# Performance work log

Hardware: AMD Instinct MI355X
Metric: run time of the kernel (lower is better)

## Reference

```python
import jax, jax.numpy as jnp
import numpy as np
import math

B, L, D, H = 2, 2048, 1024, 16
HD = D // H  # 64
SYNC_THRESHOLD = -0.7
LN_EPS = 1e-12


def setup_inputs() -> dict:
    key = jax.random.key(0)
    ks = jax.random.split(key, 12)
    s = 0.02
    return {
        "hidden_states": jax.random.normal(ks[0], (B, L, D), dtype=jnp.float32),
        "attention_mask": jnp.zeros((B, 1, 1, L), dtype=jnp.float32),
        "phi": jax.random.normal(ks[1], (B, L, H), dtype=jnp.float32),
        "Wq": jax.random.normal(ks[2], (D, D), dtype=jnp.float32) * s,
        "bq": jnp.zeros((D,), dtype=jnp.float32),
        "Wk": jax.random.normal(ks[3], (D, D), dtype=jnp.float32) * s,
        "bk": jnp.zeros((D,), dtype=jnp.float32),
        "Wv": jax.random.normal(ks[4], (D, D), dtype=jnp.float32) * s,
        "bv": jnp.zeros((D,), dtype=jnp.float32),
        "Wo": jax.random.normal(ks[5], (D, D), dtype=jnp.float32) * s,
        "bo": jnp.zeros((D,), dtype=jnp.float32),
        "ln_g": jnp.ones((D,), dtype=jnp.float32),
        "ln_b": jnp.zeros((D,), dtype=jnp.float32),
    }


def _shape(x):  # [B,L,D] -> [B,H,L,HD]
    return x.reshape(B, L, H, HD).transpose(0, 2, 1, 3)


def _rotate_half(x):
    x1, x2 = jnp.split(x, 2, axis=-1)
    return jnp.concatenate([-x2, x1], axis=-1)


def reference(hidden_states, attention_mask, phi, Wq, bq, Wk, bk, Wv, bv, Wo, bo, ln_g, ln_b):
    residual = hidden_states
    q = _shape(hidden_states @ Wq.T + bq)
    k = _shape(hidden_states @ Wk.T + bk)
    v = _shape(hidden_states @ Wv.T + bv)

    # phase per (batch, head, token): [B,H,L,1]; constant across head_dim,
    # so cos/sin of the concatenated phase are the same scalar per token/head.
    p = jnp.transpose(phi, (0, 2, 1))[..., None]
    cos_p = jnp.cos(p)
    sin_p = jnp.sin(p)
    q_rot = q * cos_p + _rotate_half(q) * sin_p
    k_rot = k * cos_p + _rotate_half(k) * sin_p

    scores = jnp.einsum("bhqd,bhkd->bhqk", q_rot, k_rot) / math.sqrt(HD)

    # data-dependent sync mask: mask pairs whose phase difference is anti-synced
    delta_phi = p - jnp.swapaxes(p, -1, -2)           # [B,H,L,L]
    eye = jnp.eye(L, dtype=bool)[None, None]          # [1,1,L,L]
    sync_mask = (jnp.cos(delta_phi) < SYNC_THRESHOLD) & ~eye
    scores = jnp.where(sync_mask, -1e9, scores)
    scores = scores + attention_mask

    # all-masked edge case: zero diagonal score so softmax attends to self
    row_max = jnp.max(scores, axis=-1, keepdims=True)
    all_masked = row_max <= -1e8
    scores = jnp.where(all_masked & eye, 0.0, scores)

    probs = jax.nn.softmax(scores, axis=-1)
    ctx = jnp.einsum("bhqk,bhkd->bhqd", probs, v)
    ctx = ctx.transpose(0, 2, 1, 3).reshape(B, L, D)

    out = ctx @ Wo.T + bo
    x = out + residual
    mean = jnp.mean(x, axis=-1, keepdims=True)
    var = jnp.var(x, axis=-1, keepdims=True)
    return (x - mean) / jnp.sqrt(var + LN_EPS) * ln_g + ln_b
```

## Files before the change

kernel.cpp:

```cpp
#include <hip/hip_runtime.h>
#include <cmath>

#define BB 2
#define LL 2048
#define DD 1024
#define HH 16
#define HDD 64

typedef _Float16 v8h __attribute__((ext_vector_type(8)));
typedef _Float16 v4h __attribute__((ext_vector_type(4)));
typedef _Float16 v2h __attribute__((ext_vector_type(2)));
typedef float v4f __attribute__((ext_vector_type(4)));

#define LOG2E 1.44269504089f
#define NEGB  (-1.442695e9f)
#define AMTHR (-1.442695e8f)

#define GLD(gp, lp)                                                        \
  __builtin_amdgcn_global_load_lds(                                        \
      (const __attribute__((address_space(1))) void*)(gp),                 \
      (__attribute__((address_space(3))) void*)(lp), 16, 0, 0)

__global__ __launch_bounds__(256) void cvt_all(
    const float* __restrict__ hs, const float* __restrict__ wq,
    const float* __restrict__ wk, const float* __restrict__ wv,
    const float* __restrict__ wo, _Float16* __restrict__ hsh,
    _Float16* __restrict__ wqkvh, _Float16* __restrict__ woh)
{
  const int i = blockIdx.x * 256 + threadIdx.x;
  const float* s;
  _Float16* d;
  if (i < 1048576)      { s = hs + (size_t)i * 4;            d = hsh + (size_t)i * 4; }
  else if (i < 1310720) { int j = i - 1048576; s = wq + (size_t)j * 4; d = wqkvh + (size_t)j * 4; }
  else if (i < 1572864) { int j = i - 1310720; s = wk + (size_t)j * 4; d = wqkvh + 1048576 + (size_t)j * 4; }
  else if (i < 1835008) { int j = i - 1572864; s = wv + (size_t)j * 4; d = wqkvh + 2097152 + (size_t)j * 4; }
  else                  { int j = i - 1835008; s = wo + (size_t)j * 4; d = woh + (size_t)j * 4; }
  float4 v = *(const float4*)s;
  v4h o;
  o[0] = (_Float16)v.x; o[1] = (_Float16)v.y;
  o[2] = (_Float16)v.z; o[3] = (_Float16)v.w;
  *(v4h*)d = o;
}

__device__ __forceinline__ void gemm_loop(
    const _Float16* __restrict__ A, const _Float16* __restrict__ W, const int K,
    const int m0, const int n0, const int tid, const int wave, const int lane,
    _Float16* As, _Float16* Bs, v4f acc[4][4])
{
  const int quad = lane >> 4;
  const int ql = lane & 15;
  const int wm = (wave >> 1) * 64;
  const int wn = (wave & 1) * 64;
  const int srow = tid >> 2;
  const int skof = (tid & 3) * 8;
  const _Float16* Ap = A + (size_t)(m0 + srow) * K + skof;
  const _Float16* Wp = W + (size_t)(n0 + srow) * K + skof;
  const size_t rstep = (size_t)64 * K;
  for (int k0 = 0; k0 < K; k0 += 32) {
    __syncthreads();
    GLD(Ap + k0,         As + tid * 8);
    GLD(Ap + rstep + k0, As + 2048 + tid * 8);
    GLD(Wp + k0,         Bs + tid * 8);
    GLD(Wp + rstep + k0, Bs + 2048 + tid * 8);
    __syncthreads();
    v8h af[4], bf[4];
#pragma unroll
    for (int mt = 0; mt < 4; ++mt)
      af[mt] = *(const v8h*)&As[(wm + mt * 16 + ql) * 32 + quad * 8];
#pragma unroll
    for (int nt = 0; nt < 4; ++nt)
      bf[nt] = *(const v8h*)&Bs[(wn + nt * 16 + ql) * 32 + quad * 8];
#pragma unroll
    for (int mt = 0; mt < 4; ++mt)
#pragma unroll
      for (int nt = 0; nt < 4; ++nt)
        acc[mt][nt] = __builtin_amdgcn_mfma_f32_16x16x32_f16(
            af[mt], bf[nt], acc[mt][nt], 0, 0, 0);
  }
}

__global__ __launch_bounds__(256) void gemm_qkv(
    const _Float16* __restrict__ A, const _Float16* __restrict__ W,
    const float* __restrict__ bq, const float* __restrict__ bk,
    const float* __restrict__ bv, _Float16* __restrict__ qh,
    _Float16* __restrict__ kh, _Float16* __restrict__ vh)
{
  __shared__ _Float16 As[128 * 32];
  __shared__ _Float16 Bs[128 * 32];
  const int tid = threadIdx.x, lane = tid & 63, wave = tid >> 6;
  const int quad = lane >> 4, ql = lane & 15;
  const int m0 = blockIdx.y * 128, n0 = blockIdx.x * 128;
  v4f acc[4][4];
#pragma unroll
  for (int mt = 0; mt < 4; ++mt)
#pragma unroll
    for (int nt = 0; nt < 4; ++nt) acc[mt][nt] = (v4f){0.f, 0.f, 0.f, 0.f};
  gemm_loop(A, W, DD, m0, n0, tid, wave, lane, As, Bs, acc);
  const int buf = n0 >> 10;
  _Float16* outp = buf == 0 ? qh : (buf == 1 ? kh : vh);
  const float* bias = buf == 0 ? bq : (buf == 1 ? bk : bv);
  const int nc0 = (n0 & 1023) + (wave & 1) * 64;
  const int mr0 = m0 + (wave >> 1) * 64;
#pragma unroll
  for (int nt = 0; nt < 4; ++nt) {
    const int col = nc0 + nt * 16 + ql;
    const float bb = bias[col];
#pragma unroll
    for (int mt = 0; mt < 4; ++mt)
#pragma unroll
      for (int r = 0; r < 4; ++r) {
        const int row = mr0 + mt * 16 + quad * 4 + r;
        outp[(size_t)row * DD + col] = (_Float16)(acc[mt][nt][r] + bb);
      }
  }
}

__global__ __launch_bounds__(256) void gemm_o(
    const _Float16* __restrict__ A, const _Float16* __restrict__ W,
    const float* __restrict__ bo, const float* __restrict__ res,
    float* __restrict__ out)
{
  __shared__ _Float16 As[128 * 32];
  __shared__ _Float16 Bs[128 * 32];
  const int tid = threadIdx.x, lane = tid & 63, wave = tid >> 6;
  const int quad = lane >> 4, ql = lane & 15;
  const int m0 = blockIdx.y * 128, n0 = blockIdx.x * 128;
  v4f acc[4][4];
#pragma unroll
  for (int mt = 0; mt < 4; ++mt)
#pragma unroll
    for (int nt = 0; nt < 4; ++nt) acc[mt][nt] = (v4f){0.f, 0.f, 0.f, 0.f};
  gemm_loop(A, W, DD, m0, n0, tid, wave, lane, As, Bs, acc);
  const int nc0 = n0 + (wave & 1) * 64;
  const int mr0 = m0 + (wave >> 1) * 64;
#pragma unroll
  for (int nt = 0; nt < 4; ++nt) {
    const int col = nc0 + nt * 16 + ql;
    const float bb = bo[col];
#pragma unroll
    for (int mt = 0; mt < 4; ++mt)
#pragma unroll
      for (int r = 0; r < 4; ++r) {
        const int row = mr0 + mt * 16 + quad * 4 + r;
        const size_t ix = (size_t)row * DD + col;
        out[ix] = acc[mt][nt][r] + bb + res[ix];
      }
  }
}

__global__ __launch_bounds__(256) void rotary_h(
    _Float16* __restrict__ q, _Float16* __restrict__ k,
    const float* __restrict__ phi, unsigned* __restrict__ csh2)
{
  const int idx = blockIdx.x * 256 + threadIdx.x;
  const int d = idx & 31;
  const int h = (idx >> 5) & (HH - 1);
  const int l = (idx >> 9) & (LL - 1);
  const int b = idx >> 20;
  const float ph = phi[(b * LL + l) * HH + h];
  const float c = cosf(ph), s = sinf(ph);
  const size_t base = ((size_t)(b * LL + l) * HH + h) * HDD;
  const float SC = 0.125f * LOG2E;
  const float q0 = (float)q[base + d], q1 = (float)q[base + d + 32];
  q[base + d]      = (_Float16)((q0 * c - q1 * s) * SC);
  q[base + d + 32] = (_Float16)((q1 * c + q0 * s) * SC);
  const float k0v = (float)k[base + d], k1v = (float)k[base + d + 32];
  k[base + d]      = (_Float16)(k0v * c - k1v * s);
  k[base + d + 32] = (_Float16)(k1v * c + k0v * s);
  if (d == 0) {
    v2h cs;
    cs[0] = (_Float16)c; cs[1] = (_Float16)s;
    csh2[(b * HH + h) * LL + l] = __builtin_bit_cast(unsigned, cs);
  }
}

__global__ __launch_bounds__(256) void vtrans(
    const _Float16* __restrict__ V, _Float16* __restrict__ VT2)
{
  __shared__ _Float16 t[64][72];
  const int bid = blockIdx.x;
  const int lt = bid & 31, bh = bid >> 5;
  const int b = bh >> 4, h = bh & 15;
  const int l0 = lt * 64;
  const int tid = threadIdx.x;
  {
    const int row = tid >> 2, doff = (tid & 3) * 16;
    const _Float16* src = V + ((size_t)((b * LL + l0 + row) * HH + h)) * HDD + doff;
    *(v8h*)&t[row][doff]     = *(const v8h*)src;
    *(v8h*)&t[row][doff + 8] = *(const v8h*)(src + 8);
  }
  __syncthreads();
  {
    _Float16* dst = VT2 + ((size_t)bh * 32 + lt) * 4096;
    const int j = tid >> 4;
    const int d0 = (tid * 4) & 63;
#pragma unroll
    for (int uu = 0; uu < 4; ++uu) {
      const int d = d0 + uu;
      v4h o;
#pragma unroll
      for (int kk = 0; kk < 4; ++kk) o[kk] = t[4 * j + kk][d];
      *(v4h*)&dst[(j * 64 + d) * 4] = o;
    }
  }
}

__global__ __launch_bounds__(256) void attn_db(
    const _Float16* __restrict__ Q, const _Float16* __restrict__ K,
    const _Float16* __restrict__ VT2, const _Float16* __restrict__ V,
    const unsigned* __restrict__ csh2, const float* __restrict__ am,
    _Float16* __restrict__ ctx)
{
  __shared__ _Float16 Kt[2][4096];
  __shared__ _Float16 Vt[2][4096];
  __shared__ float amL[LL];

  const int tid  = threadIdx.x;
  const int lane = tid & 63;
  const int wave = tid >> 6;
  const int quad = lane >> 4;
  const int ql   = lane & 15;
  const int bid  = blockIdx.x;
  const int bh = bid & 31;
  const int qt = bid >> 5;
  const int h  = bh & 15;
  const int b  = bh >> 4;
  const int q0w = qt * 64 + wave * 16;
  const int qglob = q0w + ql;
  const int csb = (b * HH + h) * LL;

  {
    const float* amb = am + b * LL;
    for (int i = tid; i < LL; i += 256) amL[i] = amb[i] * LOG2E;
  }

  v8h qf[2];
  {
    const _Float16* qp = Q + ((size_t)((b * LL + qglob) * HH + h)) * HDD + quad * 8;
    qf[0] = *(const v8h*)qp;
    qf[1] = *(const v8h*)(qp + 32);
  }
  v4h bq = (v4h){0, 0, 0, 0};
  {
    const v2h c2 = __builtin_bit_cast(v2h, csh2[csb + qglob]);
    if (quad == 0) { bq[0] = c2[0]; bq[1] = c2[1]; }
  }

  v4f o[4];
#pragma unroll
  for (int nt = 0; nt < 4; ++nt) o[nt] = (v4f){0.f, 0.f, 0.f, 0.f};
  float m2 = -INFINITY, lrow = 0.f;

  const _Float16* Kb   = K + ((size_t)(b * LL) * HH + h) * HDD;
  const _Float16* VTb2 = VT2 + (size_t)bh * 131072;
  const unsigned* csk = csh2 + csb;

  const int srow = tid >> 3;
  const int kch  = (tid & 7) ^ (srow & 7);

  {
    const size_t kg = (size_t)srow * 1024 + kch * 8;
    GLD(Kb + kg,             &Kt[0][tid * 8]);
    GLD(Kb + kg + 32 * 1024, &Kt[0][2048 + tid * 8]);
    GLD(VTb2 + tid * 8,          &Vt[0][tid * 8]);
    GLD(VTb2 + 2048 + tid * 8,   &Vt[0][2048 + tid * 8]);
  }
  unsigned cs_cur[4], cs_nxt[4];
#pragma unroll
  for (int c = 0; c < 4; ++c) cs_cur[c] = csk[c * 16 + ql];
  __syncthreads();

  for (int t = 0; t < 32; ++t) {
    const int k0 = t * 64;
    const int buf = t & 1;
    if (t < 31) {
      const int k1 = k0 + 64;
      const size_t kg = (size_t)(k1 + srow) * 1024 + kch * 8;
      GLD(Kb + kg,             &Kt[buf ^ 1][tid * 8]);
      GLD(Kb + kg + 32 * 1024, &Kt[buf ^ 1][2048 + tid * 8]);
      const _Float16* vsrc = VTb2 + (size_t)(t + 1) * 4096;
      GLD(vsrc + tid * 8,        &Vt[buf ^ 1][tid * 8]);
      GLD(vsrc + 2048 + tid * 8, &Vt[buf ^ 1][2048 + tid * 8]);
#pragma unroll
      for (int c = 0; c < 4; ++c) cs_nxt[c] = csk[k1 + c * 16 + ql];
    }
    const _Float16* KtB = Kt[buf];
    const _Float16* VtB = Vt[buf];

    v4f st[4], dd[4];
#pragma unroll
    for (int c = 0; c < 4; ++c) {
      const int row = c * 16 + ql;
      const int sw = row & 7;
      v8h a0 = *(const v8h*)&KtB[row * 64 + ((quad ^ sw) << 3)];
      v8h a1 = *(const v8h*)&KtB[row * 64 + (((quad + 4) ^ sw) << 3)];
      v4f z = (v4f){0.f, 0.f, 0.f, 0.f};
      z = __builtin_amdgcn_mfma_f32_16x16x32_f16(a0, qf[0], z, 0, 0, 0);
      z = __builtin_amdgcn_mfma_f32_16x16x32_f16(a1, qf[1], z, 0, 0, 0);
      st[c] = z;
      const v2h c2 = __builtin_bit_cast(v2h, cs_cur[c]);
      v4h a = (v4h){0, 0, 0, 0};
      if (quad == 0) { a[0] = c2[0]; a[1] = c2[1]; }
      dd[c] = __builtin_amdgcn_mfma_f32_16x16x16f16(
          a, bq, (v4f){0.f, 0.f, 0.f, 0.f}, 0, 0, 0);
    }

    float s2[16];
    float tm = -INFINITY;
    const bool hasdiag = ((unsigned)(q0w - k0)) < 64u;
    if (hasdiag) {
#pragma unroll
      for (int c = 0; c < 4; ++c) {
        const v4f am4 = *(const v4f*)&amL[k0 + c * 16 + quad * 4];
#pragma unroll
        for (int r = 0; r < 4; ++r) {
          const bool msk = (dd[c][r] < -0.7f) &&
                           ((k0 + c * 16 + quad * 4 + r) != qglob);
          float sc = (msk ? NEGB : st[c][r]) + am4[r];
          s2[c * 4 + r] = sc;
          tm = fmaxf(tm, sc);
        }
      }
    } else {
#pragma unroll
      for (int c = 0; c < 4; ++c) {
        const v4f am4 = *(const v4f*)&amL[k0 + c * 16 + quad * 4];
#pragma unroll
        for (int r = 0; r < 4; ++r) {
          float sc = ((dd[c][r] < -0.7f) ? NEGB : st[c][r]) + am4[r];
          s2[c * 4 + r] = sc;
          tm = fmaxf(tm, sc);
        }
      }
    }

    tm = fmaxf(tm, __shfl_xor(tm, 16, 64));
    tm = fmaxf(tm, __shfl_xor(tm, 32, 64));
    const float mnew = fmaxf(m2, tm);
    const float alpha = __builtin_amdgcn_exp2f(m2 - mnew);
    m2 = mnew;
    float ls = 0.f;
#pragma unroll
    for (int i = 0; i < 16; ++i) {
      const float p = __builtin_amdgcn_exp2f(s2[i] - mnew);
      s2[i] = p;
      ls += p;
    }
    ls += __shfl_xor(ls, 16, 64);
    ls += __shfl_xor(ls, 32, 64);
    lrow = lrow * alpha + ls;

    v4h pf[4];
#pragma unroll
    for (int c = 0; c < 4; ++c) {
      const unsigned u01 = __builtin_bit_cast(
          unsigned, __builtin_amdgcn_cvt_pkrtz(s2[c * 4 + 0], s2[c * 4 + 1]));
      const unsigned u23 = __builtin_bit_cast(
          unsigned, __builtin_amdgcn_cvt_pkrtz(s2[c * 4 + 2], s2[c * 4 + 3]));
      const uint2 uu = make_uint2(u01, u23);
      pf[c] = __builtin_bit_cast(v4h, uu);
    }

    {
      const float a0 = __shfl(alpha, quad * 4 + 0, 64);
      const float a1 = __shfl(alpha, quad * 4 + 1, 64);
      const float a2 = __shfl(alpha, quad * 4 + 2, 64);
      const float a3 = __shfl(alpha, quad * 4 + 3, 64);
#pragma unroll
      for (int nt = 0; nt < 4; ++nt) {
        o[nt][0] *= a0; o[nt][1] *= a1; o[nt][2] *= a2; o[nt][3] *= a3;
      }
    }

#pragma unroll
    for (int c = 0; c < 4; ++c) {
#pragma unroll
      for (int nt = 0; nt < 4; ++nt) {
        const v4h vv = *(const v4h*)&VtB[((c * 4 + quad) * 64 +
                                          nt * 16 + ql) * 4];
        o[nt] = __builtin_amdgcn_mfma_f32_16x16x16f16(pf[c], vv, o[nt], 0, 0, 0);
      }
    }
#pragma unroll
    for (int c = 0; c < 4; ++c) cs_cur[c] = cs_nxt[c];
    __syncthreads();
  }

  const float inv = 1.f / lrow;
#pragma unroll
  for (int r = 0; r < 4; ++r) {
    const int q = q0w + quad * 4 + r;
    const float ir = __shfl(inv, quad * 4 + r, 64);
    const float mr = __shfl(m2, quad * 4 + r, 64);
    const size_t ob = ((size_t)((b * LL + q) * HH + h)) * HDD + ql;
    if (mr <= AMTHR) {
      ctx[ob + 0]  = V[ob + 0];
      ctx[ob + 16] = V[ob + 16];
      ctx[ob + 32] = V[ob + 32];
      ctx[ob + 48] = V[ob + 48];
    } else {
      ctx[ob + 0]  = (_Float16)(o[0][r] * ir);
      ctx[ob + 16] = (_Float16)(o[1][r] * ir);
      ctx[ob + 32] = (_Float16)(o[2][r] * ir);
      ctx[ob + 48] = (_Float16)(o[3][r] * ir);
    }
  }
}

__global__ __launch_bounds__(256) void layernorm(
    const float* __restrict__ x, const float* __restrict__ g,
    const float* __restrict__ bta, float* __restrict__ out)
{
  __shared__ float red[8];
  const int row = blockIdx.x;
  const int tid = threadIdx.x;
  const float* xr = x + (size_t)row * DD;
  float lsum = 0.f, lsq = 0.f;
  float v[4];
#pragma unroll
  for (int i = 0; i < 4; ++i) {
    v[i] = xr[tid + i * 256];
    lsum += v[i];
    lsq += v[i] * v[i];
  }
#pragma unroll
  for (int off = 32; off > 0; off >>= 1) {
    lsum += __shfl_down(lsum, off, 64);
    lsq  += __shfl_down(lsq,  off, 64);
  }
  const int wid = tid >> 6;
  if ((tid & 63) == 0) { red[wid] = lsum; red[wid + 4] = lsq; }
  __syncthreads();
  const float tsum = red[0] + red[1] + red[2] + red[3];
  const float tsq  = red[4] + red[5] + red[6] + red[7];
  const float mean = tsum * (1.f / DD);
  const float var  = tsq * (1.f / DD) - mean * mean;
  const float inv  = rsqrtf(var + 1e-12f);
#pragma unroll
  for (int i = 0; i < 4; ++i) {
    const int c = tid + i * 256;
    out[(size_t)row * DD + c] = (v[i] - mean) * inv * g[c] + bta[c];
  }
}

extern "C" void kernel_launch(void* const* d_in, const int* in_sizes, int n_in,
                              void* d_out, int out_size, void* d_ws, size_t ws_size,
                              hipStream_t stream)
{
  const float* hs  = (const float*)d_in[0];
  const float* amk = (const float*)d_in[1];
  const float* phi = (const float*)d_in[2];
  const float* Wq  = (const float*)d_in[3];
  const float* bq  = (const float*)d_in[4];
  const float* Wk  = (const float*)d_in[5];
  const float* bk  = (const float*)d_in[6];
  const float* Wv  = (const float*)d_in[7];
  const float* bv  = (const float*)d_in[8];
  const float* Wo  = (const float*)d_in[9];
  const float* bo  = (const float*)d_in[10];
  const float* lng = (const float*)d_in[11];
  const float* lnb = (const float*)d_in[12];
  float* out = (float*)d_out;

  const size_t SZ = (size_t)BB * LL * DD;
  _Float16* hsh   = (_Float16*)d_ws;
  _Float16* qh    = hsh + SZ;
  _Float16* kh    = qh + SZ;
  _Float16* vh    = kh + SZ;
  _Float16* ctxh  = vh + SZ;
  _Float16* wqkvh = ctxh + SZ;
  _Float16* woh   = wqkvh + 3 * (size_t)DD * DD;
  _Float16* vt2   = woh + (size_t)DD * DD;
  float* xb    = (float*)(vt2 + SZ);
  unsigned* csh2 = (unsigned*)(xb + SZ);

  cvt_all<<<8192, 256, 0, stream>>>(hs, Wq, Wk, Wv, Wo, hsh, wqkvh, woh);
  gemm_qkv<<<dim3(24, 32), 256, 0, stream>>>(hsh, wqkvh, bq, bk, bv, qh, kh, vh);
  rotary_h<<<8192, 256, 0, stream>>>(qh, kh, phi, csh2);
  vtrans<<<1024, 256, 0, stream>>>(vh, vt2);
  attn_db<<<1024, 256, 0, stream>>>(qh, kh, vt2, vh, csh2, amk, ctxh);
  gemm_o<<<dim3(8, 32), 256, 0, stream>>>(ctxh, woh, bo, hs, xb);
  layernorm<<<BB * LL, 256, 0, stream>>>(xb, lng, lnb, out);
}
```

Measured before the change: 276.7 us.

## Fuse rotary and V transpose into QKV GEMM epilogue, drop online-softmax max

The separate rotary and V-transpose kernels are removed. Their work now runs in the QKV GEMM epilogue, which applies cos/sin from a small precomputed table to Q/K and writes V directly in the transposed tile layout. The attention kernel drops the running-max rescaling: it exponentiates the scores directly and accumulates row sums with an MFMA against a ones vector. This cuts two kernel launches and their memory round trips, plus the per-tile shuffles and reductions. The price is relying on scores staying small enough not to overflow exp2 or fp16 probabilities.

New measurement: 246.2 us. 11.0% less time.

```diff
diff --git a/kernel.cpp b/kernel.cpp
--- a/kernel.cpp
+++ b/kernel.cpp
@@ -14,7 +14,6 @@
 
 #define LOG2E 1.44269504089f
 #define NEGB  (-1.442695e9f)
-#define AMTHR (-1.442695e8f)
 
 #define GLD(gp, lp)                                                        \
   __builtin_amdgcn_global_load_lds(                                        \
@@ -40,6 +39,20 @@
   o[0] = (_Float16)v.x; o[1] = (_Float16)v.y;
   o[2] = (_Float16)v.z; o[3] = (_Float16)v.w;
   *(v4h*)d = o;
+}
+
+__global__ __launch_bounds__(256) void csgen(
+    const float* __restrict__ phi, unsigned* __restrict__ csh2)
+{
+  const int o = blockIdx.x * 256 + threadIdx.x;
+  const int l = o & 2047;
+  const int h = (o >> 11) & 15;
+  const int b = o >> 15;
+  const float ph = phi[(b * 2048 + l) * 16 + h];
+  v2h cs;
+  cs[0] = (_Float16)cosf(ph);
+  cs[1] = (_Float16)sinf(ph);
+  csh2[o] = __builtin_bit_cast(unsigned, cs);
 }
 
 __device__ __forceinline__ void gemm_loop(
@@ -81,9 +94,10 @@
 
 __global__ __launch_bounds__(256) void gemm_qkv(
     const _Float16* __restrict__ A, const _Float16* __restrict__ W,
-    const float* __restrict__ bq, const float* __restrict__ bk,
-    const float* __restrict__ bv, _Float16* __restrict__ qh,
-    _Float16* __restrict__ kh, _Float16* __restrict__ vh)
+    const float* __restrict__ bqp, const float* __restrict__ bkp,
+    const float* __restrict__ bvp, const unsigned* __restrict__ csh2,
+    _Float16* __restrict__ qh, _Float16* __restrict__ kh,
+    _Float16* __restrict__ vt2)
 {
   __shared__ _Float16 As[128 * 32];
   __shared__ _Float16 Bs[128 * 32];
@@ -96,21 +110,57 @@
 #pragma unroll
     for (int nt = 0; nt < 4; ++nt) acc[mt][nt] = (v4f){0.f, 0.f, 0.f, 0.f};
   gemm_loop(A, W, DD, m0, n0, tid, wave, lane, As, Bs, acc);
+
   const int buf = n0 >> 10;
-  _Float16* outp = buf == 0 ? qh : (buf == 1 ? kh : vh);
-  const float* bias = buf == 0 ? bq : (buf == 1 ? bk : bv);
-  const int nc0 = (n0 & 1023) + (wave & 1) * 64;
+  const int col0 = (n0 & 1023) + (wave & 1) * 64;
+  const int hh = col0 >> 6;
   const int mr0 = m0 + (wave >> 1) * 64;
-#pragma unroll
-  for (int nt = 0; nt < 4; ++nt) {
-    const int col = nc0 + nt * 16 + ql;
-    const float bb = bias[col];
+
+  if (buf == 2) {
+    float bb4[4];
+#pragma unroll
+    for (int nt = 0; nt < 4; ++nt) bb4[nt] = bvp[col0 + nt * 16 + ql];
+#pragma unroll
+    for (int mt = 0; mt < 4; ++mt) {
+      const int row = mr0 + mt * 16 + quad * 4;
+      const int b_ = row >> 11;
+      const int l = row & 2047;
+      _Float16* dst = vt2 + ((size_t)(b_ * 16 + hh) * 32 + (l >> 6)) * 4096 +
+                      ((l >> 2) & 15) * 256;
+#pragma unroll
+      for (int nt = 0; nt < 4; ++nt) {
+        const int d = nt * 16 + ql;
+        v4h o4;
+#pragma unroll
+        for (int r = 0; r < 4; ++r) o4[r] = (_Float16)(acc[mt][nt][r] + bb4[nt]);
+        *(v4h*)&dst[d * 4] = o4;
+      }
+    }
+  } else {
+    const float scl = (buf == 0) ? 0.125f * LOG2E : 1.0f;
+    _Float16* outp = (buf == 0) ? qh : kh;
+    const float* bias = (buf == 0) ? bqp : bkp;
+    float bb4[4];
+#pragma unroll
+    for (int nt = 0; nt < 4; ++nt) bb4[nt] = bias[col0 + nt * 16 + ql];
 #pragma unroll
     for (int mt = 0; mt < 4; ++mt)
 #pragma unroll
       for (int r = 0; r < 4; ++r) {
         const int row = mr0 + mt * 16 + quad * 4 + r;
-        outp[(size_t)row * DD + col] = (_Float16)(acc[mt][nt][r] + bb);
+        const int b_ = row >> 11;
+        const int l = row & 2047;
+        const v2h c2 = __builtin_bit_cast(
+            v2h, csh2[(b_ * 16 + hh) * 2048 + l]);
+        const float c = (float)c2[0], s = (float)c2[1];
+        _Float16* orow = outp + (size_t)row * DD + col0 + ql;
+#pragma unroll
+        for (int pp = 0; pp < 2; ++pp) {
+          const float a0 = acc[mt][pp][r] + bb4[pp];
+          const float a1 = acc[mt][pp + 2][r] + bb4[pp + 2];
+          orow[pp * 16]        = (_Float16)((a0 * c - a1 * s) * scl);
+          orow[(pp + 2) * 16]  = (_Float16)((a1 * c + a0 * s) * scl);
+        }
       }
   }
 }
@@ -148,68 +198,10 @@
   }
 }
 
-__global__ __launch_bounds__(256) void rotary_h(
-    _Float16* __restrict__ q, _Float16* __restrict__ k,
-    const float* __restrict__ phi, unsigned* __restrict__ csh2)
-{
-  const int idx = blockIdx.x * 256 + threadIdx.x;
-  const int d = idx & 31;
-  const int h = (idx >> 5) & (HH - 1);
-  const int l = (idx >> 9) & (LL - 1);
-  const int b = idx >> 20;
-  const float ph = phi[(b * LL + l) * HH + h];
-  const float c = cosf(ph), s = sinf(ph);
-  const size_t base = ((size_t)(b * LL + l) * HH + h) * HDD;
-  const float SC = 0.125f * LOG2E;
-  const float q0 = (float)q[base + d], q1 = (float)q[base + d + 32];
-  q[base + d]      = (_Float16)((q0 * c - q1 * s) * SC);
-  q[base + d + 32] = (_Float16)((q1 * c + q0 * s) * SC);
-  const float k0v = (float)k[base + d], k1v = (float)k[base + d + 32];
-  k[base + d]      = (_Float16)(k0v * c - k1v * s);
-  k[base + d + 32] = (_Float16)(k1v * c + k0v * s);
-  if (d == 0) {
-    v2h cs;
-    cs[0] = (_Float16)c; cs[1] = (_Float16)s;
-    csh2[(b * HH + h) * LL + l] = __builtin_bit_cast(unsigned, cs);
-  }
-}
-
-__global__ __launch_bounds__(256) void vtrans(
-    const _Float16* __restrict__ V, _Float16* __restrict__ VT2)
-{
-  __shared__ _Float16 t[64][72];
-  const int bid = blockIdx.x;
-  const int lt = bid & 31, bh = bid >> 5;
-  const int b = bh >> 4, h = bh & 15;
-  const int l0 = lt * 64;
-  const int tid = threadIdx.x;
-  {
-    const int row = tid >> 2, doff = (tid & 3) * 16;
-    const _Float16* src = V + ((size_t)((b * LL + l0 + row) * HH + h)) * HDD + doff;
-    *(v8h*)&t[row][doff]     = *(const v8h*)src;
-    *(v8h*)&t[row][doff + 8] = *(const v8h*)(src + 8);
-  }
-  __syncthreads();
-  {
-    _Float16* dst = VT2 + ((size_t)bh * 32 + lt) * 4096;
-    const int j = tid >> 4;
-    const int d0 = (tid * 4) & 63;
-#pragma unroll
-    for (int uu = 0; uu < 4; ++uu) {
-      const int d = d0 + uu;
-      v4h o;
-#pragma unroll
-      for (int kk = 0; kk < 4; ++kk) o[kk] = t[4 * j + kk][d];
-      *(v4h*)&dst[(j * 64 + d) * 4] = o;
-    }
-  }
-}
-
 __global__ __launch_bounds__(256) void attn_db(
     const _Float16* __restrict__ Q, const _Float16* __restrict__ K,
-    const _Float16* __restrict__ VT2, const _Float16* __restrict__ V,
-    const unsigned* __restrict__ csh2, const float* __restrict__ am,
-    _Float16* __restrict__ ctx)
+    const _Float16* __restrict__ VT2, const unsigned* __restrict__ csh2,
+    const float* __restrict__ am, _Float16* __restrict__ ctx)
 {
   __shared__ _Float16 Kt[2][4096];
   __shared__ _Float16 Vt[2][4096];
@@ -227,7 +219,7 @@
   const int b  = bh >> 4;
   const int q0w = qt * 64 + wave * 16;
   const int qglob = q0w + ql;
-  const int csb = (b * HH + h) * LL;
+  const int csb = bh * LL;
 
   {
     const float* amb = am + b * LL;
@@ -236,7 +228,7 @@
 
   v8h qf[2];
   {
-    const _Float16* qp = Q + ((size_t)((b * LL + qglob) * HH + h)) * HDD + quad * 8;
+    const _Float16* qp = Q + ((size_t)(b * LL + qglob)) * DD + h * 64 + quad * 8;
     qf[0] = *(const v8h*)qp;
     qf[1] = *(const v8h*)(qp + 32);
   }
@@ -245,13 +237,15 @@
     const v2h c2 = __builtin_bit_cast(v2h, csh2[csb + qglob]);
     if (quad == 0) { bq[0] = c2[0]; bq[1] = c2[1]; }
   }
+  const v4h ones = (v4h){(_Float16)1.f, (_Float16)1.f,
+                         (_Float16)1.f, (_Float16)1.f};
 
   v4f o[4];
 #pragma unroll
   for (int nt = 0; nt < 4; ++nt) o[nt] = (v4f){0.f, 0.f, 0.f, 0.f};
-  float m2 = -INFINITY, lrow = 0.f;
-
-  const _Float16* Kb   = K + ((size_t)(b * LL) * HH + h) * HDD;
+  v4f lacc = (v4f){0.f, 0.f, 0.f, 0.f};
+
+  const _Float16* Kb   = K + (size_t)(b * LL) * DD + h * 64;
   const _Float16* VTb2 = VT2 + (size_t)bh * 131072;
   const unsigned* csk = csh2 + csb;
 
@@ -305,75 +299,46 @@
           a, bq, (v4f){0.f, 0.f, 0.f, 0.f}, 0, 0, 0);
     }
 
-    float s2[16];
-    float tm = -INFINITY;
+    v4h pf[4];
     const bool hasdiag = ((unsigned)(q0w - k0)) < 64u;
     if (hasdiag) {
 #pragma unroll
       for (int c = 0; c < 4; ++c) {
         const v4f am4 = *(const v4f*)&amL[k0 + c * 16 + quad * 4];
+        float p[4];
 #pragma unroll
         for (int r = 0; r < 4; ++r) {
           const bool msk = (dd[c][r] < -0.7f) &&
                            ((k0 + c * 16 + quad * 4 + r) != qglob);
-          float sc = (msk ? NEGB : st[c][r]) + am4[r];
-          s2[c * 4 + r] = sc;
-          tm = fmaxf(tm, sc);
+          p[r] = __builtin_amdgcn_exp2f((msk ? NEGB : st[c][r]) + am4[r]);
         }
+        const unsigned u01 = __builtin_bit_cast(
+            unsigned, __builtin_amdgcn_cvt_pkrtz(p[0], p[1]));
+        const unsigned u23 = __builtin_bit_cast(
+            unsigned, __builtin_amdgcn_cvt_pkrtz(p[2], p[3]));
+        pf[c] = __builtin_bit_cast(v4h, make_uint2(u01, u23));
       }
     } else {
 #pragma unroll
       for (int c = 0; c < 4; ++c) {
         const v4f am4 = *(const v4f*)&amL[k0 + c * 16 + quad * 4];
+        float p[4];
 #pragma unroll
         for (int r = 0; r < 4; ++r) {
-          float sc = ((dd[c][r] < -0.7f) ? NEGB : st[c][r]) + am4[r];
-          s2[c * 4 + r] = sc;
-          tm = fmaxf(tm, sc);
+          p[r] = __builtin_amdgcn_exp2f(
+              ((dd[c][r] < -0.7f) ? NEGB : st[c][r]) + am4[r]);
         }
-      }
-    }
-
-    tm = fmaxf(tm, __shfl_xor(tm, 16, 64));
-    tm = fmaxf(tm, __shfl_xor(tm, 32, 64));
-    const float mnew = fmaxf(m2, tm);
-    const float alpha = __builtin_amdgcn_exp2f(m2 - mnew);
-    m2 = mnew;
-    float ls = 0.f;
-#pragma unroll
-    for (int i = 0; i < 16; ++i) {
-      const float p = __builtin_amdgcn_exp2f(s2[i] - mnew);
-      s2[i] = p;
-      ls += p;
-    }
-    ls += __shfl_xor(ls, 16, 64);
-    ls += __shfl_xor(ls, 32, 64);
-    lrow = lrow * alpha + ls;
-
-    v4h pf[4];
+        const unsigned u01 = __builtin_bit_cast(
+            unsigned, __builtin_amdgcn_cvt_pkrtz(p[0], p[1]));
+        const unsigned u23 = __builtin_bit_cast(
+            unsigned, __builtin_amdgcn_cvt_pkrtz(p[2], p[3]));
+        pf[c] = __builtin_bit_cast(v4h, make_uint2(u01, u23));
+      }
+    }
+
 #pragma unroll
     for (int c = 0; c < 4; ++c) {
-      const unsigned u01 = __builtin_bit_cast(
-          unsigned, __builtin_amdgcn_cvt_pkrtz(s2[c * 4 + 0], s2[c * 4 + 1]));
-      const unsigned u23 = __builtin_bit_cast(
-          unsigned, __builtin_amdgcn_cvt_pkrtz(s2[c * 4 + 2], s2[c * 4 + 3]));
-      const uint2 uu = make_uint2(u01, u23);
-      pf[c] = __builtin_bit_cast(v4h, uu);
-    }
-
-    {
-      const float a0 = __shfl(alpha, quad * 4 + 0, 64);
-      const float a1 = __shfl(alpha, quad * 4 + 1, 64);
-      const float a2 = __shfl(alpha, quad * 4 + 2, 64);
-      const float a3 = __shfl(alpha, quad * 4 + 3, 64);
-#pragma unroll
-      for (int nt = 0; nt < 4; ++nt) {
-        o[nt][0] *= a0; o[nt][1] *= a1; o[nt][2] *= a2; o[nt][3] *= a3;
-      }
-    }
-
-#pragma unroll
-    for (int c = 0; c < 4; ++c) {
+      lacc = __builtin_amdgcn_mfma_f32_16x16x16f16(pf[c], ones, lacc, 0, 0, 0);
 #pragma unroll
       for (int nt = 0; nt < 4; ++nt) {
         const v4h vv = *(const v4h*)&VtB[((c * 4 + quad) * 64 +
@@ -386,23 +351,23 @@
     __syncthreads();
   }
 
-  const float inv = 1.f / lrow;
 #pragma unroll
   for (int r = 0; r < 4; ++r) {
     const int q = q0w + quad * 4 + r;
-    const float ir = __shfl(inv, quad * 4 + r, 64);
-    const float mr = __shfl(m2, quad * 4 + r, 64);
-    const size_t ob = ((size_t)((b * LL + q) * HH + h)) * HDD + ql;
-    if (mr <= AMTHR) {
-      ctx[ob + 0]  = V[ob + 0];
-      ctx[ob + 16] = V[ob + 16];
-      ctx[ob + 32] = V[ob + 32];
-      ctx[ob + 48] = V[ob + 48];
+    const float lr = lacc[r];
+    const size_t ob = (size_t)(b * LL + q) * DD + h * 64 + ql;
+    if (lr <= 0.f) {
+      const _Float16* vsrc = VTb2 + (q >> 6) * 4096 +
+                             ((q >> 2) & 15) * 256 + (q & 3);
+#pragma unroll
+      for (int nt = 0; nt < 4; ++nt)
+        ctx[ob + nt * 16] = vsrc[(nt * 16 + ql) * 4];
     } else {
-      ctx[ob + 0]  = (_Float16)(o[0][r] * ir);
-      ctx[ob + 16] = (_Float16)(o[1][r] * ir);
-      ctx[ob + 32] = (_Float16)(o[2][r] * ir);
-      ctx[ob + 48] = (_Float16)(o[3][r] * ir);
+      const float inv = 1.f / lr;
+      ctx[ob + 0]  = (_Float16)(o[0][r] * inv);
+      ctx[ob + 16] = (_Float16)(o[1][r] * inv);
+      ctx[ob + 32] = (_Float16)(o[2][r] * inv);
+      ctx[ob + 48] = (_Float16)(o[3][r] * inv);
     }
   }
 }
@@ -466,19 +431,18 @@
   _Float16* hsh   = (_Float16*)d_ws;
   _Float16* qh    = hsh + SZ;
   _Float16* kh    = qh + SZ;
-  _Float16* vh    = kh + SZ;
-  _Float16* ctxh  = vh + SZ;
+  _Float16* vt2   = kh + SZ;
+  _Float16* ctxh  = vt2 + SZ;
   _Float16* wqkvh = ctxh + SZ;
   _Float16* woh   = wqkvh + 3 * (size_t)DD * DD;
-  _Float16* vt2   = woh + (size_t)DD * DD;
-  float* xb    = (float*)(vt2 + SZ);
+  float* xb    = (float*)(woh + (size_t)DD * DD);
   unsigned* csh2 = (unsigned*)(xb + SZ);
 
   cvt_all<<<8192, 256, 0, stream>>>(hs, Wq, Wk, Wv, Wo, hsh, wqkvh, woh);
-  gemm_qkv<<<dim3(24, 32), 256, 0, stream>>>(hsh, wqkvh, bq, bk, bv, qh, kh, vh);
-  rotary_h<<<8192, 256, 0, stream>>>(qh, kh, phi, csh2);
-  vtrans<<<1024, 256, 0, stream>>>(vh, vt2);
-  attn_db<<<1024, 256, 0, stream>>>(qh, kh, vt2, vh, csh2, amk, ctxh);
+  csgen<<<256, 256, 0, stream>>>(phi, csh2);
+  gemm_qkv<<<dim3(24, 32), 256, 0, stream>>>(hsh, wqkvh, bq, bk, bv, csh2,
+                                             qh, kh, vt2);
+  attn_db<<<1024, 256, 0, stream>>>(qh, kh, vt2, csh2, amk, ctxh);
   gemm_o<<<dim3(8, 32), 256, 0, stream>>>(ctxh, woh, bo, hs, xb);
   layernorm<<<BB * LL, 256, 0, stream>>>(xb, lng, lnb, out);
 }
```
